# Kernel optimization log

Hardware: AMD Instinct MI355X
Metric: run time of the kernel (lower is better)

## Reference

```python
import jax, jax.numpy as jnp
import numpy as np

N = 64    # input_size (number of causal nodes)
H = 512   # hidden_size
M = 64    # mediate_size
B = 1024  # batched derivative evaluations (original processes one (1,N) state at a time)


def setup_inputs() -> dict:
    key = jax.random.key(0)
    ks = jax.random.split(key, 8)
    s = lambda fan_in: 1.0 / np.sqrt(fan_in)
    x = jax.random.normal(ks[0], (B, N), dtype=jnp.float32)
    # stacked per-node weights (one set per node i in 0..N-1)
    W1 = jax.random.uniform(ks[1], (N, H, N), jnp.float32, -s(N), s(N))        # net_1 layer 1, no bias
    W2 = jax.random.uniform(ks[2], (N, M, H), jnp.float32, -s(H), s(H))        # net_1 layer 2, no bias
    W3 = jax.random.uniform(ks[3], (N, H, M + N), jnp.float32, -s(M + N), s(M + N))  # net_3 layer 1
    b3 = jax.random.uniform(ks[4], (N, H), jnp.float32, -s(M + N), s(M + N))
    W4 = jax.random.uniform(ks[5], (N, H), jnp.float32, -s(H), s(H))           # net_3 layer 2 (out dim 1)
    b4 = jax.random.uniform(ks[6], (N,), jnp.float32, -s(H), s(H))
    return {"x": x, "W1": W1, "W2": W2, "W3": W3, "b3": b3, "W4": W4, "b4": b4}


def reference(x, W1, W2, W3, b3, W4, b4):
    # Faithful DAG-case CausalDerivative.forward, batched over B states and
    # grouped over the N per-node MLPs (replacing N python-loop iterations).
    eye = jnp.eye(N, dtype=x.dtype)
    inputs_1 = x[:, None, :] * (1.0 - eye)          # (B, N, N): node i sees all-but-own value
    inputs_2 = x[:, None, :] * eye                  # (B, N, N): node i sees only own value
    h1 = jax.nn.relu(jnp.einsum('bni,nhi->bnh', inputs_1, W1))   # (B, N, H)
    r1 = jax.nn.relu(jnp.einsum('bnh,nmh->bnm', h1, W2))         # (B, N, M)
    rep3 = jnp.concatenate([r1, inputs_2], axis=-1)              # (B, N, M+N)
    h3 = jax.nn.relu(jnp.einsum('bnk,nhk->bnh', rep3, W3) + b3)  # (B, N, H)
    out = jax.nn.relu(jnp.einsum('bnh,nh->bn', h3, W4) + b4)     # (B, N) derivatives
    return out
```

## Files before the change

kernel.cpp:

```cpp
#include <hip/hip_runtime.h>

#define NN 64
#define HH 512

typedef _Float16 h8 __attribute__((ext_vector_type(8)));
typedef float    fx4 __attribute__((ext_vector_type(4)));

#define MFMA __builtin_amdgcn_mfma_f32_16x16x32_f16

#define WS_NEEDED 12713984ull

__global__ __launch_bounds__(256)
void cvt_wts(const float* __restrict__ W1, const float* __restrict__ W2,
             const float* __restrict__ W3, char* __restrict__ ws)
{
    _Float16* o1 = (_Float16*)ws;
    _Float16* o2 = o1 + 2097152;
    _Float16* o3 = o2 + 2097152;
    float*    oc = (float*)(ws + 12582912);
    const int g = blockIdx.x * 256 + threadIdx.x;

    {
        const float* s = W1 + (size_t)g * 8;
        float4 a = *(const float4*)s, b = *(const float4*)(s + 4);
        h8 h;
        h[0]=(_Float16)a.x; h[1]=(_Float16)a.y; h[2]=(_Float16)a.z; h[3]=(_Float16)a.w;
        h[4]=(_Float16)b.x; h[5]=(_Float16)b.y; h[6]=(_Float16)b.z; h[7]=(_Float16)b.w;
        *(h8*)(o1 + (size_t)g * 8) = h;
    }
    {
        const float* s = W2 + (size_t)g * 8;
        float4 a = *(const float4*)s, b = *(const float4*)(s + 4);
        h8 h;
        h[0]=(_Float16)a.x; h[1]=(_Float16)a.y; h[2]=(_Float16)a.z; h[3]=(_Float16)a.w;
        h[4]=(_Float16)b.x; h[5]=(_Float16)b.y; h[6]=(_Float16)b.z; h[7]=(_Float16)b.w;
        *(h8*)(o2 + (size_t)g * 8) = h;
    }
    {
        const int n3 = g >> 12;
        const int h3 = (g >> 3) & 511;
        const int k3 = (g & 7) * 8;
        const float* s = W3 + (size_t)n3 * 65536 + h3 * 128 + k3;
        float4 a = *(const float4*)s, b = *(const float4*)(s + 4);
        h8 h;
        h[0]=(_Float16)a.x; h[1]=(_Float16)a.y; h[2]=(_Float16)a.z; h[3]=(_Float16)a.w;
        h[4]=(_Float16)b.x; h[5]=(_Float16)b.y; h[6]=(_Float16)b.z; h[7]=(_Float16)b.w;
        *(h8*)(o3 + (size_t)g * 8) = h;
    }
    if (g < 32768) {
        const int n3 = g >> 9;
        const int h3 = g & 511;
        oc[g] = W3[(size_t)n3 * 65536 + (size_t)h3 * 128 + 64 + n3];
    }
}

__global__ __launch_bounds__(256, 2)
void causal_mfma4(const float* __restrict__ x, const char* __restrict__ ws,
                  const float* __restrict__ b3, const float* __restrict__ W4,
                  const float* __restrict__ b4, float* __restrict__ out)
{
    __shared__ __align__(16) char smem[25088];
    _Float16* priv = (_Float16*)smem;
    float*    w3cs = (float*)(smem + 18432);
    float*    b3s  = w3cs + 512;
    float*    w4s  = b3s + 512;
    float*    xns  = w4s + 512;

    const int tid  = threadIdx.x;
    const int bid  = blockIdx.x;
    const int n    = bid & 63;
    const int tile = bid >> 6;
    const int lane = tid & 63;
    const int pos  = lane & 15;
    const int quad = lane >> 4;
    const int wv   = __builtin_amdgcn_readfirstlane(tid >> 6);
    const int row0 = tile * 128;
    const int wrow = wv << 5;

    const _Float16* W1h  = (const _Float16*)ws + (size_t)n * 32768;
    const _Float16* W2h  = (const _Float16*)ws + 2097152 + (size_t)n * 32768;
    const _Float16* W3h  = (const _Float16*)ws + 4194304 + (size_t)n * 32768;
    const float*    w3cp = (const float*)(ws + 12582912) + n * 512;

    #pragma unroll
    for (int k = 0; k < 2; ++k) {
        const int h = tid + k * 256;
        w3cs[h] = w3cp[h];
        b3s[h]  = b3[n * HH + h];
        w4s[h]  = W4[n * HH + h];
    }
    if (tid < 128) xns[tid] = x[(size_t)(row0 + tid) * NN + n];

    h8 aX[2][2];
    #pragma unroll
    for (int mt = 0; mt < 2; ++mt)
        #pragma unroll
        for (int ks = 0; ks < 2; ++ks) {
            const float* p = x + (size_t)(row0 + wrow + mt * 16 + pos) * NN + ks * 32 + quad * 8;
            float4 a = *(const float4*)p, bq = *(const float4*)(p + 4);
            float v[8] = {a.x, a.y, a.z, a.w, bq.x, bq.y, bq.z, bq.w};
            const int base = ks * 32 + quad * 8;
            #pragma unroll
            for (int j = 0; j < 8; ++j) if (base + j == n) v[j] = 0.f;
            h8 h;
            #pragma unroll
            for (int j = 0; j < 8; ++j) h[j] = (_Float16)v[j];
            aX[mt][ks] = h;
        }
    __syncthreads();

    _Float16* P = priv + wv * 2304;

    fx4 acc2[2][4] = {};
    #pragma unroll 2
    for (int c = 0; c < 8; ++c) {
        const int hc = c << 6;
        fx4 accA[2][4] = {};
        #pragma unroll
        for (int ks = 0; ks < 2; ++ks)
            #pragma unroll
            for (int nt = 0; nt < 4; ++nt) {
                h8 bf = *(const h8*)(W1h + (hc + nt * 16 + pos) * 64 + ks * 32 + quad * 8);
                accA[0][nt] = MFMA(aX[0][ks], bf, accA[0][nt], 0, 0, 0);
                accA[1][nt] = MFMA(aX[1][ks], bf, accA[1][nt], 0, 0, 0);
            }
        #pragma unroll
        for (int mt = 0; mt < 2; ++mt)
            #pragma unroll
            for (int nt = 0; nt < 4; ++nt)
                #pragma unroll
                for (int r = 0; r < 4; ++r)
                    P[(mt * 16 + quad * 4 + r) * 72 + nt * 16 + pos] =
                        (_Float16)fmaxf(accA[mt][nt][r], 0.f);
        h8 aH[2][2];
        #pragma unroll
        for (int mt = 0; mt < 2; ++mt)
            #pragma unroll
            for (int ks = 0; ks < 2; ++ks)
                aH[mt][ks] = *(const h8*)(P + (mt * 16 + pos) * 72 + ks * 32 + quad * 8);
        #pragma unroll
        for (int ks = 0; ks < 2; ++ks)
            #pragma unroll
            for (int cm = 0; cm < 4; ++cm) {
                h8 bf = *(const h8*)(W2h + (cm * 16 + pos) * 512 + hc + ks * 32 + quad * 8);
                acc2[0][cm] = MFMA(aH[0][ks], bf, acc2[0][cm], 0, 0, 0);
                acc2[1][cm] = MFMA(aH[1][ks], bf, acc2[1][cm], 0, 0, 0);
            }
    }

    #pragma unroll
    for (int mt = 0; mt < 2; ++mt)
        #pragma unroll
        for (int cm = 0; cm < 4; ++cm)
            #pragma unroll
            for (int r = 0; r < 4; ++r)
                P[(mt * 16 + quad * 4 + r) * 72 + cm * 16 + pos] =
                    (_Float16)fmaxf(acc2[mt][cm][r], 0.f);
    h8 aR[2][2];
    #pragma unroll
    for (int mt = 0; mt < 2; ++mt)
        #pragma unroll
        for (int ks = 0; ks < 2; ++ks)
            aR[mt][ks] = *(const h8*)(P + (mt * 16 + pos) * 72 + ks * 32 + quad * 8);
    h8 af3[2];
    #pragma unroll
    for (int mt = 0; mt < 2; ++mt) {
        h8 h;
        #pragma unroll
        for (int j = 0; j < 8; ++j) h[j] = (_Float16)0.f;
        if (quad == 0) { h[0] = (_Float16)xns[wrow + mt * 16 + pos]; h[1] = (_Float16)1.f; }
        af3[mt] = h;
    }

    float o[2][4] = {};
    #pragma unroll 2
    for (int c = 0; c < 8; ++c) {
        const int hc = c << 6;
        fx4 acc3[2][4] = {};
        #pragma unroll
        for (int ks = 0; ks < 2; ++ks)
            #pragma unroll
            for (int nt = 0; nt < 4; ++nt) {
                h8 bf = *(const h8*)(W3h + (hc + nt * 16 + pos) * 64 + ks * 32 + quad * 8);
                acc3[0][nt] = MFMA(aR[0][ks], bf, acc3[0][nt], 0, 0, 0);
                acc3[1][nt] = MFMA(aR[1][ks], bf, acc3[1][nt], 0, 0, 0);
            }
        #pragma unroll
        for (int nt = 0; nt < 4; ++nt) {
            h8 bf3;
            #pragma unroll
            for (int j = 0; j < 8; ++j) bf3[j] = (_Float16)0.f;
            if (quad == 0) {
                const int h = hc + nt * 16 + pos;
                bf3[0] = (_Float16)w3cs[h];
                bf3[1] = (_Float16)b3s[h];
            }
            acc3[0][nt] = MFMA(af3[0], bf3, acc3[0][nt], 0, 0, 0);
            acc3[1][nt] = MFMA(af3[1], bf3, acc3[1][nt], 0, 0, 0);
        }
        #pragma unroll
        for (int nt = 0; nt < 4; ++nt) {
            const float w4v = w4s[hc + nt * 16 + pos];
            #pragma unroll
            for (int mt = 0; mt < 2; ++mt)
                #pragma unroll
                for (int r = 0; r < 4; ++r)
                    o[mt][r] = fmaf(fmaxf(acc3[mt][nt][r], 0.f), w4v, o[mt][r]);
        }
    }

    #pragma unroll
    for (int m = 1; m < 16; m <<= 1)
        #pragma unroll
        for (int mt = 0; mt < 2; ++mt)
            #pragma unroll
            for (int r = 0; r < 4; ++r)
                o[mt][r] += __shfl_xor(o[mt][r], m, 64);

    if (pos == 0) {
        const float bb = b4[n];
        #pragma unroll
        for (int mt = 0; mt < 2; ++mt)
            #pragma unroll
            for (int r = 0; r < 4; ++r) {
                const int row = row0 + wrow + mt * 16 + quad * 4 + r;
                out[(size_t)row * 64 + n] = fmaxf(o[mt][r] + bb, 0.f);
            }
    }
}

__device__ __forceinline__ void cvt_store16(_Float16* d, const float4* p) {
    h8 h0, h1;
    h0[0]=(_Float16)p[0].x; h0[1]=(_Float16)p[0].y; h0[2]=(_Float16)p[0].z; h0[3]=(_Float16)p[0].w;
    h0[4]=(_Float16)p[1].x; h0[5]=(_Float16)p[1].y; h0[6]=(_Float16)p[1].z; h0[7]=(_Float16)p[1].w;
    h1[0]=(_Float16)p[2].x; h1[1]=(_Float16)p[2].y; h1[2]=(_Float16)p[2].z; h1[3]=(_Float16)p[2].w;
    h1[4]=(_Float16)p[3].x; h1[5]=(_Float16)p[3].y; h1[6]=(_Float16)p[3].z; h1[7]=(_Float16)p[3].w;
    *(h8*)d = h0; *((h8*)d + 1) = h1;
}

__global__ __launch_bounds__(256, 2)
void causal_mfma3(const float* __restrict__ x,  const float* __restrict__ W1,
                  const float* __restrict__ W2, const float* __restrict__ W3,
                  const float* __restrict__ b3, const float* __restrict__ W4,
                  const float* __restrict__ b4, float* __restrict__ out)
{
    __shared__ __align__(16) char smem[61952];
    _Float16* W1c  = (_Float16*)smem;
    _Float16* W2c  = W1c + 2 * 4608;
    _Float16* priv = W2c + 2 * 4608;
    float*    w3cs = (float*)(smem + 55296);
    float*    b3s  = w3cs + 512;
    float*    w4s  = b3s + 512;
    float*    xns  = w4s + 512;

    const int tid  = threadIdx.x;
    const int bid  = blockIdx.x;
    const int n    = bid & 63;
    const int tile = bid >> 6;
    const int lane = tid & 63;
    const int pos  = lane & 15;
    const int quad = lane >> 4;
    const int wv   = __builtin_amdgcn_readfirstlane(tid >> 6);
    const int row0 = tile * 128;
    const int wrow = wv << 5;

    const float* W1n = W1 + (size_t)n * HH * NN;
    const float* W2n = W2 + (size_t)n * NN * HH;
    const float* W3n = W3 + (size_t)n * HH * 128;

    const int trow = tid >> 2;
    const int tcol = (tid & 3) << 4;

    {
        float4 p1[4], p2[4];
        #pragma unroll
        for (int q = 0; q < 4; ++q) p1[q] = *(const float4*)(W1n + trow * 64 + tcol + q * 4);
        #pragma unroll
        for (int q = 0; q < 4; ++q) p2[q] = *(const float4*)(W2n + (size_t)trow * HH + tcol + q * 4);
        #pragma unroll
        for (int k = 0; k < 2; ++k) {
            const int h = tid + k * 256;
            w3cs[h] = W3n[(size_t)h * 128 + 64 + n];
            b3s[h]  = b3[n * HH + h];
            w4s[h]  = W4[n * HH + h];
        }
        if (tid < 128) xns[tid] = x[(size_t)(row0 + tid) * NN + n];
        cvt_store16(W1c + trow * 72 + tcol, p1);
        cvt_store16(W2c + trow * 72 + tcol, p2);
    }

    h8 aX[2][2];
    #pragma unroll
    for (int mt = 0; mt < 2; ++mt)
        #pragma unroll
        for (int ks = 0; ks < 2; ++ks) {
            const float* p = x + (size_t)(row0 + wrow + mt * 16 + pos) * NN + ks * 32 + quad * 8;
            float4 a = *(const float4*)p, bq = *(const float4*)(p + 4);
            float v[8] = {a.x, a.y, a.z, a.w, bq.x, bq.y, bq.z, bq.w};
            const int base = ks * 32 + quad * 8;
            #pragma unroll
            for (int j = 0; j < 8; ++j) if (base + j == n) v[j] = 0.f;
            h8 h;
            #pragma unroll
            for (int j = 0; j < 8; ++j) h[j] = (_Float16)v[j];
            aX[mt][ks] = h;
        }
    __syncthreads();

    _Float16* P = priv + wv * 2304;

    fx4 acc2[2][4] = {};
    for (int c = 0; c < 8; ++c) {
        const int cb = c & 1;
        float4 p1[4], p2[4];
        if (c < 7) {
            const int hb1 = (c + 1) << 6;
            #pragma unroll
            for (int q = 0; q < 4; ++q) p1[q] = *(const float4*)(W1n + (hb1 + trow) * 64 + tcol + q * 4);
            #pragma unroll
            for (int q = 0; q < 4; ++q) p2[q] = *(const float4*)(W2n + (size_t)trow * HH + hb1 + tcol + q * 4);
        }
        const _Float16* W1L = W1c + cb * 4608;
        fx4 accA[2][4] = {};
        #pragma unroll
        for (int ks = 0; ks < 2; ++ks)
            #pragma unroll
            for (int nt = 0; nt < 4; ++nt) {
                h8 bf = *(const h8*)(W1L + (nt * 16 + pos) * 72 + ks * 32 + quad * 8);
                accA[0][nt] = MFMA(aX[0][ks], bf, accA[0][nt], 0, 0, 0);
                accA[1][nt] = MFMA(aX[1][ks], bf, accA[1][nt], 0, 0, 0);
            }
        #pragma unroll
        for (int mt = 0; mt < 2; ++mt)
            #pragma unroll
            for (int nt = 0; nt < 4; ++nt)
                #pragma unroll
                for (int r = 0; r < 4; ++r)
                    P[(mt * 16 + quad * 4 + r) * 72 + nt * 16 + pos] =
                        (_Float16)fmaxf(accA[mt][nt][r], 0.f);
        h8 aH[2][2];
        #pragma unroll
        for (int mt = 0; mt < 2; ++mt)
            #pragma unroll
            for (int ks = 0; ks < 2; ++ks)
                aH[mt][ks] = *(const h8*)(P + (mt * 16 + pos) * 72 + ks * 32 + quad * 8);
        const _Float16* W2L = W2c + cb * 4608;
        #pragma unroll
        for (int ks = 0; ks < 2; ++ks)
            #pragma unroll
            for (int cm = 0; cm < 4; ++cm) {
                h8 bf = *(const h8*)(W2L + (cm * 16 + pos) * 72 + ks * 32 + quad * 8);
                acc2[0][cm] = MFMA(aH[0][ks], bf, acc2[0][cm], 0, 0, 0);
                acc2[1][cm] = MFMA(aH[1][ks], bf, acc2[1][cm], 0, 0, 0);
            }
        if (c < 7) {
            cvt_store16(W1c + (cb ^ 1) * 4608 + trow * 72 + tcol, p1);
            cvt_store16(W2c + (cb ^ 1) * 4608 + trow * 72 + tcol, p2);
        }
        __syncthreads();
    }

    #pragma unroll
    for (int mt = 0; mt < 2; ++mt)
        #pragma unroll
        for (int cm = 0; cm < 4; ++cm)
            #pragma unroll
            for (int r = 0; r < 4; ++r)
                P[(mt * 16 + quad * 4 + r) * 72 + cm * 16 + pos] =
                    (_Float16)fmaxf(acc2[mt][cm][r], 0.f);
    h8 aR[2][2];
    #pragma unroll
    for (int mt = 0; mt < 2; ++mt)
        #pragma unroll
        for (int ks = 0; ks < 2; ++ks)
            aR[mt][ks] = *(const h8*)(P + (mt * 16 + pos) * 72 + ks * 32 + quad * 8);
    h8 af3[2];
    #pragma unroll
    for (int mt = 0; mt < 2; ++mt) {
        h8 h;
        #pragma unroll
        for (int j = 0; j < 8; ++j) h[j] = (_Float16)0.f;
        if (quad == 0) { h[0] = (_Float16)xns[wrow + mt * 16 + pos]; h[1] = (_Float16)1.f; }
        af3[mt] = h;
    }

    {
        float4 p3[4];
        #pragma unroll
        for (int q = 0; q < 4; ++q) p3[q] = *(const float4*)(W3n + (size_t)trow * 128 + tcol + q * 4);
        cvt_store16(W1c + trow * 72 + tcol, p3);
    }
    __syncthreads();

    float o[2][4] = {};
    for (int c = 0; c < 8; ++c) {
        const int cb = c & 1;
        const int hc = c << 6;
        float4 p3[4];
        if (c < 7) {
            #pragma unroll
            for (int q = 0; q < 4; ++q)
                p3[q] = *(const float4*)(W3n + (size_t)(hc + 64 + trow) * 128 + tcol + q * 4);
        }
        const _Float16* W3L = W1c + cb * 4608;
        fx4 acc3[2][4] = {};
        #pragma unroll
        for (int ks = 0; ks < 2; ++ks)
            #pragma unroll
            for (int nt = 0; nt < 4; ++nt) {
                h8 bf = *(const h8*)(W3L + (nt * 16 + pos) * 72 + ks * 32 + quad * 8);
                acc3[0][nt] = MFMA(aR[0][ks], bf, acc3[0][nt], 0, 0, 0);
                acc3[1][nt] = MFMA(aR[1][ks], bf, acc3[1][nt], 0, 0, 0);
            }
        #pragma unroll
        for (int nt = 0; nt < 4; ++nt) {
            h8 bf3;
            #pragma unroll
            for (int j = 0; j < 8; ++j) bf3[j] = (_Float16)0.f;
            if (quad == 0) {
                const int h = hc + nt * 16 + pos;
                bf3[0] = (_Float16)w3cs[h];
                bf3[1] = (_Float16)b3s[h];
            }
            acc3[0][nt] = MFMA(af3[0], bf3, acc3[0][nt], 0, 0, 0);
            acc3[1][nt] = MFMA(af3[1], bf3, acc3[1][nt], 0, 0, 0);
        }
        #pragma unroll
        for (int nt = 0; nt < 4; ++nt) {
            const float w4v = w4s[hc + nt * 16 + pos];
            #pragma unroll
            for (int mt = 0; mt < 2; ++mt)
                #pragma unroll
                for (int r = 0; r < 4; ++r)
                    o[mt][r] = fmaf(fmaxf(acc3[mt][nt][r], 0.f), w4v, o[mt][r]);
        }
        if (c < 7) cvt_store16(W1c + (cb ^ 1) * 4608 + trow * 72 + tcol, p3);
        __syncthreads();
    }

    #pragma unroll
    for (int m = 1; m < 16; m <<= 1)
        #pragma unroll
        for (int mt = 0; mt < 2; ++mt)
            #pragma unroll
            for (int r = 0; r < 4; ++r)
                o[mt][r] += __shfl_xor(o[mt][r], m, 64);

    if (pos == 0) {
        const float bb = b4[n];
        #pragma unroll
        for (int mt = 0; mt < 2; ++mt)
            #pragma unroll
            for (int r = 0; r < 4; ++r) {
                const int row = row0 + wrow + mt * 16 + quad * 4 + r;
                out[(size_t)row * 64 + n] = fmaxf(o[mt][r] + bb, 0.f);
            }
    }
}

extern "C" void kernel_launch(void* const* d_in, const int* in_sizes, int n_in,
                              void* d_out, int out_size, void* d_ws, size_t ws_size,
                              hipStream_t stream)
{
    const float* x  = (const float*)d_in[0];
    const float* W1 = (const float*)d_in[1];
    const float* W2 = (const float*)d_in[2];
    const float* W3 = (const float*)d_in[3];
    const float* b3 = (const float*)d_in[4];
    const float* W4 = (const float*)d_in[5];
    const float* b4 = (const float*)d_in[6];
    float* out = (float*)d_out;

    if (d_ws != nullptr && ws_size >= WS_NEEDED) {
        hipLaunchKernelGGL(cvt_wts, dim3(1024), dim3(256), 0, stream,
                           W1, W2, W3, (char*)d_ws);
        hipLaunchKernelGGL(causal_mfma4, dim3(512), dim3(256), 0, stream,
                           x, (const char*)d_ws, b3, W4, b4, out);
    } else {
        hipLaunchKernelGGL(causal_mfma3, dim3(512), dim3(256), 0, stream,
                           x, W1, W2, W3, b3, W4, b4, out);
    }
}
```

Baseline: 136.7 us.

## Pre-swizzle weights into MFMA fragment order and double-buffer them in LDS

The conversion kernel now writes W1/W2/W3 in MFMA B-fragment order, so each lane's 16-byte fragment is contiguous. The main kernel stages each 64-row weight chunk into LDS with global_load_lds, double-buffered so the next chunk loads while the current one is used. Each wave's fragments are then read from LDS with simple indexing instead of strided global loads. The cost is more LDS per block (about 57KB, which may limit two blocks per CU), a __syncthreads per chunk iteration, and the removal of the unroll-2 hints.

```diff
diff --git a/kernel.cpp b/kernel.cpp
--- a/kernel.cpp
+++ b/kernel.cpp
@@ -10,42 +10,56 @@
 
 #define WS_NEEDED 12713984ull
 
+typedef __attribute__((address_space(1))) const unsigned int gu32;
+typedef __attribute__((address_space(3))) unsigned int       lu32;
+
+__device__ __forceinline__ void gld16(const void* g, void* l) {
+    __builtin_amdgcn_global_load_lds((gu32*)g, (lu32*)l, 16, 0, 0);
+}
+
+__device__ __forceinline__ h8 cvt8(const float* __restrict__ s) {
+    float4 a = *(const float4*)s, b = *(const float4*)(s + 4);
+    h8 h;
+    h[0]=(_Float16)a.x; h[1]=(_Float16)a.y; h[2]=(_Float16)a.z; h[3]=(_Float16)a.w;
+    h[4]=(_Float16)b.x; h[5]=(_Float16)b.y; h[6]=(_Float16)b.z; h[7]=(_Float16)b.w;
+    return h;
+}
+
 __global__ __launch_bounds__(256)
-void cvt_wts(const float* __restrict__ W1, const float* __restrict__ W2,
-             const float* __restrict__ W3, char* __restrict__ ws)
+void cvt_frag(const float* __restrict__ W1, const float* __restrict__ W2,
+              const float* __restrict__ W3, char* __restrict__ ws)
 {
+    const int g    = blockIdx.x * 256 + threadIdx.x;
+    const int n    = g >> 12;
+    const int c    = (g >> 9) & 7;
+    const int ks   = (g >> 8) & 1;
+    const int nt   = (g >> 6) & 3;
+    const int l    = g & 63;
+    const int pos  = l & 15;
+    const int quad = l >> 4;
+
     _Float16* o1 = (_Float16*)ws;
     _Float16* o2 = o1 + 2097152;
     _Float16* o3 = o2 + 2097152;
     float*    oc = (float*)(ws + 12582912);
-    const int g = blockIdx.x * 256 + threadIdx.x;
 
     {
-        const float* s = W1 + (size_t)g * 8;
-        float4 a = *(const float4*)s, b = *(const float4*)(s + 4);
-        h8 h;
-        h[0]=(_Float16)a.x; h[1]=(_Float16)a.y; h[2]=(_Float16)a.z; h[3]=(_Float16)a.w;
-        h[4]=(_Float16)b.x; h[5]=(_Float16)b.y; h[6]=(_Float16)b.z; h[7]=(_Float16)b.w;
-        *(h8*)(o1 + (size_t)g * 8) = h;
+        const float* s = W1 + (size_t)n * 32768
+                            + (size_t)(c * 64 + nt * 16 + pos) * 64
+                            + ks * 32 + quad * 8;
+        *(h8*)(o1 + (size_t)g * 8) = cvt8(s);
     }
     {
-        const float* s = W2 + (size_t)g * 8;
-        float4 a = *(const float4*)s, b = *(const float4*)(s + 4);
-        h8 h;
-        h[0]=(_Float16)a.x; h[1]=(_Float16)a.y; h[2]=(_Float16)a.z; h[3]=(_Float16)a.w;
-        h[4]=(_Float16)b.x; h[5]=(_Float16)b.y; h[6]=(_Float16)b.z; h[7]=(_Float16)b.w;
-        *(h8*)(o2 + (size_t)g * 8) = h;
+        const float* s = W2 + (size_t)n * 32768
+                            + (size_t)(nt * 16 + pos) * 512
+                            + c * 64 + ks * 32 + quad * 8;
+        *(h8*)(o2 + (size_t)g * 8) = cvt8(s);
     }
     {
-        const int n3 = g >> 12;
-        const int h3 = (g >> 3) & 511;
-        const int k3 = (g & 7) * 8;
-        const float* s = W3 + (size_t)n3 * 65536 + h3 * 128 + k3;
-        float4 a = *(const float4*)s, b = *(const float4*)(s + 4);
-        h8 h;
-        h[0]=(_Float16)a.x; h[1]=(_Float16)a.y; h[2]=(_Float16)a.z; h[3]=(_Float16)a.w;
-        h[4]=(_Float16)b.x; h[5]=(_Float16)b.y; h[6]=(_Float16)b.z; h[7]=(_Float16)b.w;
-        *(h8*)(o3 + (size_t)g * 8) = h;
+        const float* s = W3 + (size_t)n * 65536
+                            + (size_t)(c * 64 + nt * 16 + pos) * 128
+                            + ks * 32 + quad * 8;
+        *(h8*)(o3 + (size_t)g * 8) = cvt8(s);
     }
     if (g < 32768) {
         const int n3 = g >> 9;
@@ -55,13 +69,15 @@
 }
 
 __global__ __launch_bounds__(256, 2)
-void causal_mfma4(const float* __restrict__ x, const char* __restrict__ ws,
+void causal_mfma5(const float* __restrict__ x, const char* __restrict__ ws,
                   const float* __restrict__ b3, const float* __restrict__ W4,
                   const float* __restrict__ b4, float* __restrict__ out)
 {
-    __shared__ __align__(16) char smem[25088];
-    _Float16* priv = (_Float16*)smem;
-    float*    w3cs = (float*)(smem + 18432);
+    __shared__ __align__(16) char smem[57856];
+    _Float16* w1b  = (_Float16*)smem;
+    _Float16* w2b  = w1b + 8192;
+    _Float16* priv = w2b + 8192;
+    float*    w3cs = (float*)(smem + 51200);
     float*    b3s  = w3cs + 512;
     float*    w4s  = b3s + 512;
     float*    xns  = w4s + 512;
@@ -77,11 +93,19 @@
     const int row0 = tile * 128;
     const int wrow = wv << 5;
 
-    const _Float16* W1h  = (const _Float16*)ws + (size_t)n * 32768;
-    const _Float16* W2h  = (const _Float16*)ws + 2097152 + (size_t)n * 32768;
-    const _Float16* W3h  = (const _Float16*)ws + 4194304 + (size_t)n * 32768;
+    const _Float16* W1f  = (const _Float16*)ws + (size_t)n * 32768;
+    const _Float16* W2f  = (const _Float16*)ws + 2097152 + (size_t)n * 32768;
+    const _Float16* W3f  = (const _Float16*)ws + 4194304 + (size_t)n * 32768;
     const float*    w3cp = (const float*)(ws + 12582912) + n * 512;
 
+    {
+        const _Float16* s1 = W1f + wv * 1024 + lane * 8;
+        gld16(s1,       w1b + wv * 1024);
+        gld16(s1 + 512, w1b + wv * 1024 + 512);
+        const _Float16* s2 = W2f + wv * 1024 + lane * 8;
+        gld16(s2,       w2b + wv * 1024);
+        gld16(s2 + 512, w2b + wv * 1024 + 512);
+    }
     #pragma unroll
     for (int k = 0; k < 2; ++k) {
         const int h = tid + k * 256;
@@ -112,15 +136,27 @@
     _Float16* P = priv + wv * 2304;
 
     fx4 acc2[2][4] = {};
-    #pragma unroll 2
     for (int c = 0; c < 8; ++c) {
-        const int hc = c << 6;
+        const int cb = c & 1;
+        if (c < 7) {
+            const _Float16* s1 = W1f + (c + 1) * 4096 + wv * 1024 + lane * 8;
+            gld16(s1,       w1b + (cb ^ 1) * 4096 + wv * 1024);
+            gld16(s1 + 512, w1b + (cb ^ 1) * 4096 + wv * 1024 + 512);
+            const _Float16* s2 = W2f + (c + 1) * 4096 + wv * 1024 + lane * 8;
+            gld16(s2,       w2b + (cb ^ 1) * 4096 + wv * 1024);
+            gld16(s2 + 512, w2b + (cb ^ 1) * 4096 + wv * 1024 + 512);
+        } else {
+            const _Float16* s3 = W3f + wv * 1024 + lane * 8;
+            gld16(s3,       w1b + wv * 1024);
+            gld16(s3 + 512, w1b + wv * 1024 + 512);
+        }
+        const h8* F1 = (const h8*)(w1b + cb * 4096);
         fx4 accA[2][4] = {};
         #pragma unroll
         for (int ks = 0; ks < 2; ++ks)
             #pragma unroll
             for (int nt = 0; nt < 4; ++nt) {
-                h8 bf = *(const h8*)(W1h + (hc + nt * 16 + pos) * 64 + ks * 32 + quad * 8);
+                h8 bf = F1[(ks * 4 + nt) * 64 + lane];
                 accA[0][nt] = MFMA(aX[0][ks], bf, accA[0][nt], 0, 0, 0);
                 accA[1][nt] = MFMA(aX[1][ks], bf, accA[1][nt], 0, 0, 0);
             }
@@ -138,14 +174,16 @@
             #pragma unroll
             for (int ks = 0; ks < 2; ++ks)
                 aH[mt][ks] = *(const h8*)(P + (mt * 16 + pos) * 72 + ks * 32 + quad * 8);
+        const h8* F2 = (const h8*)(w2b + cb * 4096);
         #pragma unroll
         for (int ks = 0; ks < 2; ++ks)
             #pragma unroll
             for (int cm = 0; cm < 4; ++cm) {
-                h8 bf = *(const h8*)(W2h + (cm * 16 + pos) * 512 + hc + ks * 32 + quad * 8);
+                h8 bf = F2[(ks * 4 + cm) * 64 + lane];
                 acc2[0][cm] = MFMA(aH[0][ks], bf, acc2[0][cm], 0, 0, 0);
                 acc2[1][cm] = MFMA(aH[1][ks], bf, acc2[1][cm], 0, 0, 0);
             }
+        __syncthreads();
     }
 
     #pragma unroll
@@ -173,15 +211,21 @@
     }
 
     float o[2][4] = {};
-    #pragma unroll 2
     for (int c = 0; c < 8; ++c) {
+        const int cb = c & 1;
         const int hc = c << 6;
+        if (c < 7) {
+            const _Float16* s3 = W3f + (c + 1) * 4096 + wv * 1024 + lane * 8;
+            gld16(s3,       w1b + (cb ^ 1) * 4096 + wv * 1024);
+            gld16(s3 + 512, w1b + (cb ^ 1) * 4096 + wv * 1024 + 512);
+        }
+        const h8* F3 = (const h8*)(w1b + cb * 4096);
         fx4 acc3[2][4] = {};
         #pragma unroll
         for (int ks = 0; ks < 2; ++ks)
             #pragma unroll
             for (int nt = 0; nt < 4; ++nt) {
-                h8 bf = *(const h8*)(W3h + (hc + nt * 16 + pos) * 64 + ks * 32 + quad * 8);
+                h8 bf = F3[(ks * 4 + nt) * 64 + lane];
                 acc3[0][nt] = MFMA(aR[0][ks], bf, acc3[0][nt], 0, 0, 0);
                 acc3[1][nt] = MFMA(aR[1][ks], bf, acc3[1][nt], 0, 0, 0);
             }
@@ -207,6 +251,7 @@
                 for (int r = 0; r < 4; ++r)
                     o[mt][r] = fmaf(fmaxf(acc3[mt][nt][r], 0.f), w4v, o[mt][r]);
         }
+        __syncthreads();
     }
 
     #pragma unroll
@@ -472,9 +517,9 @@
     float* out = (float*)d_out;
 
     if (d_ws != nullptr && ws_size >= WS_NEEDED) {
-        hipLaunchKernelGGL(cvt_wts, dim3(1024), dim3(256), 0, stream,
+        hipLaunchKernelGGL(cvt_frag, dim3(1024), dim3(256), 0, stream,
                            W1, W2, W3, (char*)d_ws);
-        hipLaunchKernelGGL(causal_mfma4, dim3(512), dim3(256), 0, stream,
+        hipLaunchKernelGGL(causal_mfma5, dim3(512), dim3(256), 0, stream,
                            x, (const char*)d_ws, b3, W4, b4, out);
     } else {
         hipLaunchKernelGGL(causal_mfma3, dim3(512), dim3(256), 0, stream,
```

Result: faster. 112.7 us (-17.6%).
